# Performance work log

Measured on AMD Instinct MI355X. Metric: run time of the kernel, lower is better.

Reference implementation:

```python
import jax, jax.numpy as jnp
import numpy as np

N_ENT = 100000
N_REL = 1000
RANK = 256
B = 1024
MAX_NB = 50


def setup_inputs() -> dict:
    key = jax.random.key(0)
    ks = jax.random.split(key, 12)
    s = 0.001  # init_size scaling as in the torch module
    x = jax.random.randint(ks[0], (B, 3), 0, N_REL)  # in-range for ents and rels
    nb_idx = jax.random.randint(ks[1], (B, MAX_NB), 0, N_ENT)
    lhs_w = jax.random.normal(ks[2], (N_ENT, RANK), jnp.float32) * s
    rel_w = jax.random.normal(ks[3], (N_REL, RANK), jnp.float32) * s
    rhs_w = jax.random.normal(ks[4], (N_ENT, RANK), jnp.float32) * s
    W_w = jax.random.normal(ks[5], (RANK, 2 * RANK), jnp.float32) * 0.05
    W_b = jnp.zeros((RANK,), jnp.float32)
    W2_w = jax.random.normal(ks[6], (RANK, RANK), jnp.float32) * 0.05
    W2_b = jnp.zeros((RANK,), jnp.float32)
    Wo_w = jax.random.normal(ks[7], (1, RANK), jnp.float32) * 0.05
    Wo_b = jnp.zeros((1,), jnp.float32)
    Uo_w = jax.random.normal(ks[8], (1, RANK), jnp.float32) * 0.05
    Uo_b = jnp.zeros((1,), jnp.float32)
    return dict(x=x, nb_idx=nb_idx, lhs_w=lhs_w, rel_w=rel_w, rhs_w=rhs_w,
                W_w=W_w, W_b=W_b, W2_w=W2_w, W2_b=W2_b,
                Wo_w=Wo_w, Wo_b=Wo_b, Uo_w=Uo_w, Uo_b=Uo_b)


def reference(x, nb_idx, lhs_w, rel_w, rhs_w, W_w, W_b, W2_w, W2_b, Wo_w, Wo_b, Uo_w, Uo_b):
    lhs = lhs_w[x[:, 0]]            # [B, r]
    rel = rel_w[x[:, 1]]            # [B, r]
    rhs = rhs_w[x[:, 2]]            # [B, r]
    trp_E = jnp.concatenate([lhs, rel], axis=1)          # [B, 2r]
    w = trp_E @ W_w.T + W_b                               # [B, r]
    nb_E = rhs_w[nb_idx]                                  # [B, M, r] irregular gather
    alpha = jax.nn.softmax(jnp.einsum('bk,bmk->bm', w, nb_E), axis=1)
    e_c = jnp.einsum('bm,bmk->bk', alpha, nb_E) @ W2_w.T + W2_b  # [B, r]
    g = jax.nn.sigmoid((lhs * rel) @ Uo_w.T + Uo_b + e_c @ Wo_w.T + Wo_b)  # [B, 1]
    gated_e_c = g * e_c + (1.0 - g)                       # [B, r]
    tot_forward = (lhs * rel * gated_e_c) @ rhs_w.T       # [B, n_ent]
    return tot_forward, (lhs, rel, rhs, e_c)
```

## Files before the change

kernel.cpp:

```cpp
#include <hip/hip_runtime.h>
#include <hip/hip_bf16.h>

#define B_TRIPLES 1024
#define N_ENT 100000
#define RANK 256
#define MAX_NB 50

typedef float f32x4 __attribute__((ext_vector_type(4)));
typedef __bf16 bf16x8 __attribute__((ext_vector_type(8)));

__device__ __forceinline__ unsigned short f32_to_bf16_bits(float f) {
    unsigned u = __float_as_uint(f);
    unsigned r = ((u >> 16) & 1u) + 0x7fffu;
    return (unsigned short)((u + r) >> 16);
}

__global__ __launch_bounds__(256) void prep_kernel(
    const float* __restrict__ W_w, const float* __restrict__ W2_w,
    float* __restrict__ Wt4, float* __restrict__ W2t4)
{
    int t = blockIdx.x * 256 + threadIdx.x;
    if (t < RANK * 2 * RANK) {
        int k = t >> 9, j = t & 511;
        Wt4[((j >> 2) * RANK + k) * 4 + (j & 3)] = W_w[t];
    } else {
        int u = t - RANK * 2 * RANK;
        int k = u >> 8, j = u & 255;
        W2t4[((j >> 2) * RANK + k) * 4 + (j & 3)] = W2_w[u];
    }
}

__global__ __launch_bounds__(256) void triple_kernel(
    const int* __restrict__ x, const int* __restrict__ nb_idx,
    const float* __restrict__ lhs_w, const float* __restrict__ rel_w,
    const float* __restrict__ rhs_w,
    const float* __restrict__ Wt4, const float* __restrict__ W_b,
    const float* __restrict__ W2t4, const float* __restrict__ W2_b,
    const float* __restrict__ Wo_w, const float* __restrict__ Wo_b,
    const float* __restrict__ Uo_w, const float* __restrict__ Uo_b,
    float* __restrict__ out_tail, unsigned short* __restrict__ qb)
{
    __shared__ float trp[2 * RANK];
    __shared__ float w_s[RANK];
    __shared__ float alpha_s[MAX_NB];
    __shared__ int   nbrow[MAX_NB];
    __shared__ float red[8];

    const int b    = blockIdx.x;
    const int k    = threadIdx.x;
    const int lane = k & 63;
    const int wv   = k >> 6;

    const int i0 = x[b * 3 + 0];
    const int i1 = x[b * 3 + 1];
    const int i2 = x[b * 3 + 2];

    const float lhs  = lhs_w[(size_t)i0 * RANK + k];
    const float rel  = rel_w[(size_t)i1 * RANK + k];
    const float rhsv = rhs_w[(size_t)i2 * RANK + k];

    out_tail[0 * B_TRIPLES * RANK + b * RANK + k] = lhs;
    out_tail[1 * B_TRIPLES * RANK + b * RANK + k] = rel;
    out_tail[2 * B_TRIPLES * RANK + b * RANK + k] = rhsv;

    trp[k]        = lhs;
    trp[RANK + k] = rel;
    if (k < MAX_NB) nbrow[k] = nb_idx[b * MAX_NB + k];
    __syncthreads();

    float acc = W_b[k];
    {
        const float4* Wp = (const float4*)Wt4;
        #pragma unroll 8
        for (int jc = 0; jc < (2 * RANK) / 4; ++jc) {
            float4 wv4 = Wp[jc * RANK + k];
            float4 t   = *(const float4*)&trp[jc * 4];
            acc += wv4.x * t.x + wv4.y * t.y + wv4.z * t.z + wv4.w * t.w;
        }
    }
    w_s[k] = acc;
    __syncthreads();

    for (int m = wv; m < MAX_NB; m += 4) {
        const float* nrow = rhs_w + (size_t)nbrow[m] * RANK;
        float4 nv  = *(const float4*)(nrow + lane * 4);
        float4 wv4 = *(const float4*)(w_s + lane * 4);
        float p = nv.x * wv4.x + nv.y * wv4.y + nv.z * wv4.z + nv.w * wv4.w;
        #pragma unroll
        for (int off = 32; off > 0; off >>= 1) p += __shfl_down(p, off);
        if (lane == 0) alpha_s[m] = p;
    }
    __syncthreads();

    if (wv == 0) {
        float v = (lane < MAX_NB) ? alpha_s[lane] : -1e30f;
        float mx = v;
        #pragma unroll
        for (int off = 1; off < 64; off <<= 1) mx = fmaxf(mx, __shfl_xor(mx, off));
        float e = (lane < MAX_NB) ? __expf(v - mx) : 0.f;
        float s = e;
        #pragma unroll
        for (int off = 1; off < 64; off <<= 1) s += __shfl_xor(s, off);
        if (lane < MAX_NB) alpha_s[lane] = e / s;
    }
    __syncthreads();

    float ecp = 0.f;
    #pragma unroll 5
    for (int m = 0; m < MAX_NB; ++m)
        ecp += alpha_s[m] * rhs_w[(size_t)nbrow[m] * RANK + k];
    trp[k] = ecp;
    __syncthreads();

    float ec = W2_b[k];
    {
        const float4* W2p = (const float4*)W2t4;
        #pragma unroll 8
        for (int jc = 0; jc < RANK / 4; ++jc) {
            float4 wv4 = W2p[jc * RANK + k];
            float4 t   = *(const float4*)&trp[jc * 4];
            ec += wv4.x * t.x + wv4.y * t.y + wv4.z * t.z + wv4.w * t.w;
        }
    }
    out_tail[3 * B_TRIPLES * RANK + b * RANK + k] = ec;

    float part = lhs * rel * Uo_w[k] + ec * Wo_w[k];
    #pragma unroll
    for (int off = 32; off > 0; off >>= 1) part += __shfl_down(part, off);
    if (lane == 0) red[wv] = part;
    __syncthreads();
    if (k == 0) {
        float s = red[0] + red[1] + red[2] + red[3] + Uo_b[0] + Wo_b[0];
        red[4] = 1.f / (1.f + __expf(-s));
    }
    __syncthreads();
    const float g = red[4];
    const float gated = g * ec + (1.f - g);
    qb[b * RANK + k] = f32_to_bf16_bits(lhs * rel * gated);
}

__global__ __launch_bounds__(256) void cvt_kernel(
    const float* __restrict__ in, unsigned short* __restrict__ outp)
{
    size_t t = (size_t)blockIdx.x * 256 + threadIdx.x;
    const float4* p = (const float4*)in + 2 * t;
    float4 a = p[0], c = p[1];
    uint4 o;
    o.x = (unsigned)f32_to_bf16_bits(a.x) | ((unsigned)f32_to_bf16_bits(a.y) << 16);
    o.y = (unsigned)f32_to_bf16_bits(a.z) | ((unsigned)f32_to_bf16_bits(a.w) << 16);
    o.z = (unsigned)f32_to_bf16_bits(c.x) | ((unsigned)f32_to_bf16_bits(c.y) << 16);
    o.w = (unsigned)f32_to_bf16_bits(c.z) | ((unsigned)f32_to_bf16_bits(c.w) << 16);
    ((uint4*)outp)[t] = o;
}

__global__ __launch_bounds__(512) void gemm_kernel(
    const unsigned short* __restrict__ rhsb,
    const unsigned short* __restrict__ qb,
    float* __restrict__ out)
{
    const int lane = threadIdx.x & 63;
    const int wv   = threadIdx.x >> 6;
    const int r    = lane & 15;
    const int quad = lane >> 4;

    const int bid = blockIdx.x;
    constexpr int Q = 390, R = 6;
    const int xcd = bid & 7, off = bid >> 3;
    const int swz = (xcd < R ? xcd * (Q + 1) : R * (Q + 1) + (xcd - R) * Q) + off;

    const int e_blk  = (swz >> 1) * 64;
    const int b_base = (swz & 1) * 512 + wv * 64;

    f32x4 acc[4][4] = {};

    #pragma unroll
    for (int kt = 0; kt < 8; ++kt) {
        const int ko = kt * 32 + quad * 8;
        union { uint4 u; bf16x8 v; } a[4], bb[4];
        #pragma unroll
        for (int tm = 0; tm < 4; ++tm) {
            const int brow = b_base + tm * 16 + r;
            a[tm].u = *(const uint4*)(qb + (size_t)brow * RANK + ko);
        }
        #pragma unroll
        for (int tn = 0; tn < 4; ++tn) {
            int e = e_blk + tn * 16 + r;
            if (e >= N_ENT) e = N_ENT - 1;
            bb[tn].u = *(const uint4*)(rhsb + (size_t)e * RANK + ko);
        }
        #pragma unroll
        for (int tm = 0; tm < 4; ++tm)
            #pragma unroll
            for (int tn = 0; tn < 4; ++tn)
                acc[tm][tn] = __builtin_amdgcn_mfma_f32_16x16x32_bf16(
                    a[tm].v, bb[tn].v, acc[tm][tn], 0, 0, 0);
    }

    #pragma unroll
    for (int tm = 0; tm < 4; ++tm) {
        #pragma unroll
        for (int i = 0; i < 4; ++i) {
            const int brow = b_base + tm * 16 + quad * 4 + i;
            float* orow = out + (size_t)brow * N_ENT;
            #pragma unroll
            for (int tn = 0; tn < 4; ++tn) {
                const int e = e_blk + tn * 16 + r;
                if (e < N_ENT) orow[e] = acc[tm][tn][i];
            }
        }
    }
}

extern "C" void kernel_launch(void* const* d_in, const int* in_sizes, int n_in,
                              void* d_out, int out_size, void* d_ws, size_t ws_size,
                              hipStream_t stream)
{
    const int*   x     = (const int*)d_in[0];
    const int*   nb    = (const int*)d_in[1];
    const float* lhs_w = (const float*)d_in[2];
    const float* rel_w = (const float*)d_in[3];
    const float* rhs_w = (const float*)d_in[4];
    const float* W_w   = (const float*)d_in[5];
    const float* W_b   = (const float*)d_in[6];
    const float* W2_w  = (const float*)d_in[7];
    const float* W2_b  = (const float*)d_in[8];
    const float* Wo_w  = (const float*)d_in[9];
    const float* Wo_b  = (const float*)d_in[10];
    const float* Uo_w  = (const float*)d_in[11];
    const float* Uo_b  = (const float*)d_in[12];

    float* out      = (float*)d_out;
    float* out_tail = out + (size_t)B_TRIPLES * N_ENT;

    unsigned short* rhsb = (unsigned short*)d_ws;
    unsigned short* qb   = rhsb + (size_t)N_ENT * RANK;
    float* Wt4  = (float*)(qb + (size_t)B_TRIPLES * RANK);
    float* W2t4 = Wt4 + (size_t)(2 * RANK) * RANK;

    prep_kernel<<<768, 256, 0, stream>>>(W_w, W2_w, Wt4, W2t4);

    triple_kernel<<<B_TRIPLES, 256, 0, stream>>>(
        x, nb, lhs_w, rel_w, rhs_w, Wt4, W_b, W2t4, W2_b,
        Wo_w, Wo_b, Uo_w, Uo_b, out_tail, qb);

    cvt_kernel<<<12500, 256, 0, stream>>>(rhs_w, rhsb);

    gemm_kernel<<<3126, 512, 0, stream>>>(rhsb, qb, out);

    (void)in_sizes; (void)n_in; (void)out_size; (void)ws_size;
}
```

Baseline: 748.3 us.

## Fuse fp32-to-bf16 conversion of rhs_w into GEMM and use nontemporal output stores

Removes the separate conversion kernel that turned the whole rhs_w table into bf16 in workspace, and instead has the GEMM load fp32 rows and convert them to bf16 in registers before the MFMA. This saves a full read and write pass over the 100k x 256 table plus one kernel launch. In exchange, each GEMM block reads twice as many bytes for its B operand, and rows are re-read by both batch-half blocks. Output stores also become nontemporal so the large 1024x100000 result streams past the cache.

```diff
diff --git a/kernel.cpp b/kernel.cpp
--- a/kernel.cpp
+++ b/kernel.cpp
@@ -139,22 +139,8 @@
     qb[b * RANK + k] = f32_to_bf16_bits(lhs * rel * gated);
 }
 
-__global__ __launch_bounds__(256) void cvt_kernel(
-    const float* __restrict__ in, unsigned short* __restrict__ outp)
-{
-    size_t t = (size_t)blockIdx.x * 256 + threadIdx.x;
-    const float4* p = (const float4*)in + 2 * t;
-    float4 a = p[0], c = p[1];
-    uint4 o;
-    o.x = (unsigned)f32_to_bf16_bits(a.x) | ((unsigned)f32_to_bf16_bits(a.y) << 16);
-    o.y = (unsigned)f32_to_bf16_bits(a.z) | ((unsigned)f32_to_bf16_bits(a.w) << 16);
-    o.z = (unsigned)f32_to_bf16_bits(c.x) | ((unsigned)f32_to_bf16_bits(c.y) << 16);
-    o.w = (unsigned)f32_to_bf16_bits(c.z) | ((unsigned)f32_to_bf16_bits(c.w) << 16);
-    ((uint4*)outp)[t] = o;
-}
-
 __global__ __launch_bounds__(512) void gemm_kernel(
-    const unsigned short* __restrict__ rhsb,
+    const float* __restrict__ rhs_w,
     const unsigned short* __restrict__ qb,
     float* __restrict__ out)
 {
@@ -186,7 +172,12 @@
         for (int tn = 0; tn < 4; ++tn) {
             int e = e_blk + tn * 16 + r;
             if (e >= N_ENT) e = N_ENT - 1;
-            bb[tn].u = *(const uint4*)(rhsb + (size_t)e * RANK + ko);
+            const float4* pr = (const float4*)(rhs_w + (size_t)e * RANK + ko);
+            float4 b0 = pr[0], b1 = pr[1];
+            bb[tn].u.x = (unsigned)f32_to_bf16_bits(b0.x) | ((unsigned)f32_to_bf16_bits(b0.y) << 16);
+            bb[tn].u.y = (unsigned)f32_to_bf16_bits(b0.z) | ((unsigned)f32_to_bf16_bits(b0.w) << 16);
+            bb[tn].u.z = (unsigned)f32_to_bf16_bits(b1.x) | ((unsigned)f32_to_bf16_bits(b1.y) << 16);
+            bb[tn].u.w = (unsigned)f32_to_bf16_bits(b1.z) | ((unsigned)f32_to_bf16_bits(b1.w) << 16);
         }
         #pragma unroll
         for (int tm = 0; tm < 4; ++tm)
@@ -205,7 +196,8 @@
             #pragma unroll
             for (int tn = 0; tn < 4; ++tn) {
                 const int e = e_blk + tn * 16 + r;
-                if (e < N_ENT) orow[e] = acc[tm][tn][i];
+                if (e < N_ENT)
+                    __builtin_nontemporal_store(acc[tm][tn][i], &orow[e]);
             }
         }
     }
@@ -232,8 +224,7 @@
     float* out      = (float*)d_out;
     float* out_tail = out + (size_t)B_TRIPLES * N_ENT;
 
-    unsigned short* rhsb = (unsigned short*)d_ws;
-    unsigned short* qb   = rhsb + (size_t)N_ENT * RANK;
+    unsigned short* qb = (unsigned short*)d_ws;
     float* Wt4  = (float*)(qb + (size_t)B_TRIPLES * RANK);
     float* W2t4 = Wt4 + (size_t)(2 * RANK) * RANK;
 
@@ -243,9 +234,7 @@
         x, nb, lhs_w, rel_w, rhs_w, Wt4, W_b, W2t4, W2_b,
         Wo_w, Wo_b, Uo_w, Uo_b, out_tail, qb);
 
-    cvt_kernel<<<12500, 256, 0, stream>>>(rhs_w, rhsb);
-
-    gemm_kernel<<<3126, 512, 0, stream>>>(rhsb, qb, out);
+    gemm_kernel<<<3126, 512, 0, stream>>>(rhs_w, qb, out);
 
     (void)in_sizes; (void)n_in; (void)out_size; (void)ws_size;
 }
```

Result: slower. 859.5 us (+14.9%).

## Pre-tile bf16 operands into MFMA fragment layout for contiguous GEMM loads

Applied to the files above, without the earlier changes.

The bf16 conversion kernel now stages 16-row tiles of rhs_w in shared memory and writes them in a tiled layout where each 16-entity by 8-k fragment is contiguous. The query vector q is written in the same tiled layout by the triple kernel. The GEMM then loads each MFMA operand fragment as one contiguous 256-byte chunk per wave instead of 16 strided rows, which should improve load coalescing. This adds an LDS staging pass in the conversion kernel and changes the launch order so the conversion runs first.

```diff
diff --git a/kernel.cpp b/kernel.cpp
--- a/kernel.cpp
+++ b/kernel.cpp
@@ -5,6 +5,7 @@
 #define N_ENT 100000
 #define RANK 256
 #define MAX_NB 50
+#define N_ETILE (N_ENT / 16)
 
 typedef float f32x4 __attribute__((ext_vector_type(4)));
 typedef __bf16 bf16x8 __attribute__((ext_vector_type(8)));
@@ -13,6 +14,9 @@
     unsigned u = __float_as_uint(f);
     unsigned r = ((u >> 16) & 1u) + 0x7fffu;
     return (unsigned short)((u + r) >> 16);
+}
+__device__ __forceinline__ unsigned pack2(float a, float b) {
+    return (unsigned)f32_to_bf16_bits(a) | ((unsigned)f32_to_bf16_bits(b) << 16);
 }
 
 __global__ __launch_bounds__(256) void prep_kernel(
@@ -27,6 +31,35 @@
         int u = t - RANK * 2 * RANK;
         int k = u >> 8, j = u & 255;
         W2t4[((j >> 2) * RANK + k) * 4 + (j & 3)] = W2_w[u];
+    }
+}
+
+__global__ __launch_bounds__(256) void cvt_kernel(
+    const float* __restrict__ in, unsigned short* __restrict__ outp)
+{
+    __shared__ float lds[16 * 264];
+    const int tile = blockIdx.x;
+    const int t = threadIdx.x;
+    const float4* src = (const float4*)(in + (size_t)tile * 16 * RANK);
+    #pragma unroll
+    for (int p = 0; p < 4; ++p) {
+        int u = t + 256 * p;
+        int row = u >> 6, c4 = u & 63;
+        *(float4*)&lds[row * 264 + c4 * 4] = src[u];
+    }
+    __syncthreads();
+    uint4* dst = (uint4*)outp + (size_t)tile * 512;
+    #pragma unroll
+    for (int p = 0; p < 2; ++p) {
+        int u2 = t + 256 * p;
+        int e_local = u2 & 15, kg = u2 >> 4;
+        const float* s = &lds[e_local * 264 + kg * 8];
+        uint4 o;
+        o.x = pack2(s[0], s[1]);
+        o.y = pack2(s[2], s[3]);
+        o.z = pack2(s[4], s[5]);
+        o.w = pack2(s[6], s[7]);
+        dst[u2] = o;
     }
 }
 
@@ -136,26 +169,13 @@
     __syncthreads();
     const float g = red[4];
     const float gated = g * ec + (1.f - g);
-    qb[b * RANK + k] = f32_to_bf16_bits(lhs * rel * gated);
-}
-
-__global__ __launch_bounds__(256) void cvt_kernel(
-    const float* __restrict__ in, unsigned short* __restrict__ outp)
-{
-    size_t t = (size_t)blockIdx.x * 256 + threadIdx.x;
-    const float4* p = (const float4*)in + 2 * t;
-    float4 a = p[0], c = p[1];
-    uint4 o;
-    o.x = (unsigned)f32_to_bf16_bits(a.x) | ((unsigned)f32_to_bf16_bits(a.y) << 16);
-    o.y = (unsigned)f32_to_bf16_bits(a.z) | ((unsigned)f32_to_bf16_bits(a.w) << 16);
-    o.z = (unsigned)f32_to_bf16_bits(c.x) | ((unsigned)f32_to_bf16_bits(c.y) << 16);
-    o.w = (unsigned)f32_to_bf16_bits(c.z) | ((unsigned)f32_to_bf16_bits(c.w) << 16);
-    ((uint4*)outp)[t] = o;
+    qb[(((size_t)(b >> 4) * 32 + (k >> 3)) * 16 + (b & 15)) * 8 + (k & 7)] =
+        f32_to_bf16_bits(lhs * rel * gated);
 }
 
 __global__ __launch_bounds__(512) void gemm_kernel(
-    const unsigned short* __restrict__ rhsb,
-    const unsigned short* __restrict__ qb,
+    const unsigned short* __restrict__ rhsp,
+    const unsigned short* __restrict__ qp,
     float* __restrict__ out)
 {
     const int lane = threadIdx.x & 63;
@@ -168,25 +188,24 @@
     const int xcd = bid & 7, off = bid >> 3;
     const int swz = (xcd < R ? xcd * (Q + 1) : R * (Q + 1) + (xcd - R) * Q) + off;
 
-    const int e_blk  = (swz >> 1) * 64;
+    const int et64   = swz >> 1;
     const int b_base = (swz & 1) * 512 + wv * 64;
+    const int btile  = b_base >> 4;
 
     f32x4 acc[4][4] = {};
 
     #pragma unroll
     for (int kt = 0; kt < 8; ++kt) {
-        const int ko = kt * 32 + quad * 8;
+        const int kq = kt * 4 + quad;
         union { uint4 u; bf16x8 v; } a[4], bb[4];
         #pragma unroll
-        for (int tm = 0; tm < 4; ++tm) {
-            const int brow = b_base + tm * 16 + r;
-            a[tm].u = *(const uint4*)(qb + (size_t)brow * RANK + ko);
-        }
+        for (int tm = 0; tm < 4; ++tm)
+            a[tm].u = *(const uint4*)(qp + ((size_t)((btile + tm) * 32 + kq) * 16 + r) * 8);
         #pragma unroll
         for (int tn = 0; tn < 4; ++tn) {
-            int e = e_blk + tn * 16 + r;
-            if (e >= N_ENT) e = N_ENT - 1;
-            bb[tn].u = *(const uint4*)(rhsb + (size_t)e * RANK + ko);
+            int etile = et64 * 4 + tn;
+            if (etile >= N_ETILE) etile = N_ETILE - 1;
+            bb[tn].u = *(const uint4*)(rhsp + ((size_t)(etile * 32 + kq) * 16 + r) * 8);
         }
         #pragma unroll
         for (int tm = 0; tm < 4; ++tm)
@@ -196,6 +215,7 @@
                     a[tm].v, bb[tn].v, acc[tm][tn], 0, 0, 0);
     }
 
+    const int e_blk = et64 * 64;
     #pragma unroll
     for (int tm = 0; tm < 4; ++tm) {
         #pragma unroll
@@ -232,20 +252,20 @@
     float* out      = (float*)d_out;
     float* out_tail = out + (size_t)B_TRIPLES * N_ENT;
 
-    unsigned short* rhsb = (unsigned short*)d_ws;
-    unsigned short* qb   = rhsb + (size_t)N_ENT * RANK;
-    float* Wt4  = (float*)(qb + (size_t)B_TRIPLES * RANK);
+    unsigned short* rhsp = (unsigned short*)d_ws;
+    unsigned short* qp   = rhsp + (size_t)N_ENT * RANK;
+    float* Wt4  = (float*)(qp + (size_t)B_TRIPLES * RANK);
     float* W2t4 = Wt4 + (size_t)(2 * RANK) * RANK;
+
+    cvt_kernel<<<N_ETILE, 256, 0, stream>>>(rhs_w, rhsp);
 
     prep_kernel<<<768, 256, 0, stream>>>(W_w, W2_w, Wt4, W2t4);
 
     triple_kernel<<<B_TRIPLES, 256, 0, stream>>>(
         x, nb, lhs_w, rel_w, rhs_w, Wt4, W_b, W2t4, W2_b,
-        Wo_w, Wo_b, Uo_w, Uo_b, out_tail, qb);
-
-    cvt_kernel<<<12500, 256, 0, stream>>>(rhs_w, rhsb);
-
-    gemm_kernel<<<3126, 512, 0, stream>>>(rhsb, qb, out);
+        Wo_w, Wo_b, Uo_w, Uo_b, out_tail, qp);
+
+    gemm_kernel<<<3126, 512, 0, stream>>>(rhsp, qp, out);
 
     (void)in_sizes; (void)n_in; (void)out_size; (void)ws_size;
 }
```

New measurement: 672.7 us. 10.1% less time.
